# Optimization experiments

Hardware: AMD Instinct MI355X
Metric: run time of the kernel (lower is better)

The kernel has to match this reference:

```python
import jax, jax.numpy as jnp
import numpy as np

STRIDE = 1  # conv stride from __init__


def setup_inputs() -> dict:
    key = jax.random.key(0)
    k1, k2, k3 = jax.random.split(key, 3)
    prot1 = jax.random.normal(k1, (4, 1024, 8, 64), dtype=jnp.float32)
    prot2 = jax.random.normal(k2, (4, 1024, 8, 64), dtype=jnp.float32)
    # W: (no_filters, no_channels, no_dims, window_size)
    W = jax.random.normal(k3, (32, 8, 64, 7), dtype=jnp.float32)
    return {"prot1": prot1, "prot2": prot2, "W": W}


def _project(x, W, stride):
    """Fused equivalent of unfold + broadcast-mul + sum over (C, window).

    x: (N, H, C, D), W: (F, C, D, w) -> (N, F, H', D) with H' = (H - w)//stride + 1.
    This is a grouped 1D conv: D groups, each mixing C input channels into F outputs.
    """
    N, H, C, D = x.shape
    Fn, _, _, w = W.shape
    xg = jnp.transpose(x, (0, 3, 2, 1)).reshape(N, D * C, H)        # (N, D*C, H)
    Wg = jnp.transpose(W, (2, 0, 1, 3)).reshape(D * Fn, C, w)       # (D*F, C, w)
    out = jax.lax.conv_general_dilated(
        xg, Wg, window_strides=(stride,), padding='VALID',
        dimension_numbers=('NCH', 'OIH', 'NCH'), feature_group_count=D)
    Hp = out.shape[-1]
    return jnp.transpose(out.reshape(N, D, Fn, Hp), (0, 2, 3, 1))   # (N, F, H', D)


def reference(prot1, prot2, W):
    q1 = _project(prot1, W, STRIDE)   # (N, F, H1', D)
    q2 = _project(prot2, W, STRIDE)   # (N, F, H2', D)
    H1p, H2p = q1.shape[2], q2.shape[2]
    scale = jnp.sqrt(jnp.asarray(H1p * H2p, dtype=q1.dtype))
    att = jnp.einsum('nfhd,nfgd->nfhg', q1, q2) / scale             # (N, F, H1', H2')
    a = jax.nn.softmax(att, axis=3)
    p1 = jnp.einsum('nfhg,nfgd->nfhd', a, q2)                       # (N, F, H1', D)
    # NB: source does transpose(att, 2, 2) (a no-op) and multiplies the SAME
    # softmax matrix by the UPDATED p1folds; we reproduce that faithfully.
    p2 = jnp.einsum('nfhg,nfgd->nfhd', a, p1)                       # (N, F, H1', D)
    out1 = jnp.tanh(jnp.transpose(p1, (0, 2, 1, 3)))                # (N, H1', F, D)
    out2 = jnp.tanh(jnp.transpose(p2, (0, 2, 1, 3)))
    # Dropout is identity in eval mode (and dropout_p=0.0 here).
    return (out1, out2)
```

## Files before the change

### kernel.cpp

```cpp
#include <hip/hip_runtime.h>
#include <math.h>

typedef __bf16 bf16_t;
typedef bf16_t bf16x4 __attribute__((ext_vector_type(4)));
typedef bf16_t bf16x8 __attribute__((ext_vector_type(8)));
typedef float  f32x16 __attribute__((ext_vector_type(16)));

#define HH 1024
#define CC 8
#define DD 64
#define FF 32
#define WW 7
#define HP 1018
#define HPAD 1024
#define NF 128
#define QOUT (NF*HP*DD)
#define QWS ((size_t)NF*HPAD*DD)
#define SCEXP (1.442695041f/1018.f)

#if __has_builtin(__builtin_amdgcn_exp2f)
#define EXP2(x) __builtin_amdgcn_exp2f(x)
#else
#define EXP2(x) __expf((x) * 0.6931471805599453f)
#endif

__device__ __forceinline__ int vaddr(int row, int col) {
    return row*64 + ((((col>>3) ^ (row&7) ^ ((row>>2)&7)))<<3) + (col&7);
}

__global__ __launch_bounds__(256) void wprep_kernel(
    const float* __restrict__ Wt, float* __restrict__ Wp)
{
    const int idx = blockIdx.x * 256 + threadIdx.x;
    if (idx < FF*CC*DD*WW) {
        const int j = idx % WW;
        int t = idx / WW;
        const int d = t % DD; t /= DD;
        const int c = t % CC;
        const int f = t / CC;
        Wp[((f*CC + c)*WW + j)*DD + d] = Wt[idx];
    }
}

__global__ __launch_bounds__(256) void xprep_kernel(
    const float* __restrict__ x1, const float* __restrict__ x2,
    bf16_t* __restrict__ xt)
{
    __shared__ float ls[8][CC][DD+1];
    const float* x = blockIdx.z ? x2 : x1;
    bf16_t* o = xt + (size_t)blockIdx.z * (4*HH*512);
    const int n = blockIdx.y;
    const int r0 = blockIdx.x * 8;
    const int tid = threadIdx.x;

#pragma unroll
    for (int it = 0; it < 4; ++it) {
        const int i = it*256 + tid;
        const int r = i >> 7;
        const int idx = i & 127;
        const int c = idx >> 4;
        const int d0 = (idx & 15) * 4;
        float4 v = *(const float4*)&x[((size_t)(n*HH + r0 + r)*CC + c)*DD + d0];
        ls[r][c][d0+0] = v.x; ls[r][c][d0+1] = v.y;
        ls[r][c][d0+2] = v.z; ls[r][c][d0+3] = v.w;
    }
    __syncthreads();
    const int d = tid & 63;
    for (int r = (tid >> 6); r < 8; r += 4) {
        bf16_t tmp[8];
#pragma unroll
        for (int c = 0; c < CC; ++c) tmp[c] = (bf16_t)ls[r][c][d];
        *(bf16x8*)&o[((size_t)(n*HH + r0 + r)*DD + d)*CC] = *(bf16x8*)tmp;
    }
}

__global__ __launch_bounds__(256) void conv_kernel(
    const bf16_t* __restrict__ xt, const float* __restrict__ Wp,
    bf16_t* __restrict__ q1, bf16_t* __restrict__ q2)
{
    __shared__ __align__(16) bf16_t xs[22*64*8];
    const int z = blockIdx.z;
    const bf16_t* xb = xt + (size_t)z * (4*HH*512);
    bf16_t* q = z ? q2 : q1;
    const float qscale = z ? 1.0f : SCEXP;
    const int n = blockIdx.y;
    const int hb = blockIdx.x * 16;
    const int tid = threadIdx.x;

    for (int i = tid; i < 22*64; i += 256) {
        const int row = hb + (i >> 6);
        const int dd = i & 63;
        bf16x8 v = {};
        if (row < HH) v = *(const bf16x8*)&xb[((size_t)(n*HH + row)*DD + dd)*CC];
        *(bf16x8*)&xs[(size_t)i*8] = v;
    }
    __syncthreads();

    const int d = tid & 63;
    const int fq = tid >> 6;
    for (int fi = 0; fi < 8; ++fi) {
        const int f = fq*8 + fi;
        float w[CC][WW];
#pragma unroll
        for (int c = 0; c < CC; ++c)
#pragma unroll
            for (int j = 0; j < WW; ++j)
                w[c][j] = Wp[((f*CC + c)*WW + j)*DD + d];
        float acc[16];
#pragma unroll
        for (int i = 0; i < 16; ++i) acc[i] = 0.f;
#pragma unroll
        for (int rr = 0; rr < 22; ++rr) {
            bf16x8 xv8 = *(const bf16x8*)&xs[(rr*64 + d)*8];
            float xv[8];
#pragma unroll
            for (int c = 0; c < CC; ++c) xv[c] = (float)xv8[c];
#pragma unroll
            for (int j = 0; j < WW; ++j) {
                const int i = rr - j;
                if (i >= 0 && i < 16) {
#pragma unroll
                    for (int c = 0; c < CC; ++c)
                        acc[i] = fmaf(xv[c], w[c][j], acc[i]);
                }
            }
        }
#pragma unroll
        for (int i = 0; i < 16; ++i) {
            const int h = hb + i;
            const float v = (h < HP) ? acc[i] * qscale : 0.f;
            q[((size_t)(n*FF + f)*HPAD + h)*DD + d] = (bf16_t)v;
        }
    }
}

__device__ __forceinline__ float fast_tanh(float x) {
    const float t = __expf(2.f * x);
    return (t - 1.f) / (t + 1.f);
}

template<int MODE>
__global__ __launch_bounds__(256, 2) void flash(
    const bf16_t* __restrict__ q1, const bf16_t* __restrict__ q2,
    const bf16_t* __restrict__ vsrc, bf16_t* __restrict__ p1out,
    float* __restrict__ out)
{
    __shared__ __align__(16) bf16_t Vt[64*64];

    const int head = blockIdx.y;
    const int n = head >> 5, f = head & 31;
    const int tid = threadIdx.x;
    const int w = tid >> 6;
    const int lane = tid & 63;
    const int lid = lane & 31;
    const int half = lane >> 5;
    const int hb = blockIdx.x * 256 + w * 64;

    const size_t qoff = (size_t)head * HPAD * DD;
    const int vswz = (lid & 7) ^ (lid >> 2);

    const int gq = tid >> 4;
    const int dq = tid & 15;
    const int cgb = 4*((gq>>1)&1) + 8*(gq&1) + 16*(gq>>2);

    const bf16_t* vptr = (MODE == 1) ? vsrc : q2;

    bf16x8 bq1[2][4];
#pragma unroll
    for (int nt = 0; nt < 2; ++nt)
#pragma unroll
        for (int kt = 0; kt < 4; ++kt)
            bq1[nt][kt] = *(const bf16x8*)&q1[qoff + (size_t)(hb + 32*nt + lid)*DD + 16*kt + 8*half];

    bf16x8 onesb;
#pragma unroll
    for (int j = 0; j < 8; ++j) onesb[j] = (bf16_t)1.0f;

    bf16x8 aq[2][4];
#pragma unroll
    for (int mt = 0; mt < 2; ++mt)
#pragma unroll
        for (int kt = 0; kt < 4; ++kt)
            aq[mt][kt] = *(const bf16x8*)&q2[qoff + (size_t)(32*mt + lid)*DD + 16*kt + 8*half];

    bf16x4 rV[4];
#pragma unroll
    for (int i = 0; i < 4; ++i)
        rV[i] = *(const bf16x4*)&vptr[qoff + (size_t)(4*gq + i)*DD + 4*dq];

    f32x16 O[2][2] = {};
    f32x16 lO[2] = {};

    for (int g0 = 0; g0 < HPAD; g0 += 64) {
        __syncthreads();
#pragma unroll
        for (int j = 0; j < 4; ++j) {
            bf16x4 c = { rV[0][j], rV[1][j], rV[2][j], rV[3][j] };
            *(bf16x4*)&Vt[vaddr(4*dq + j, cgb)] = c;
        }
        __syncthreads();

        if (g0 + 64 < HPAD) {
#pragma unroll
            for (int i = 0; i < 4; ++i)
                rV[i] = *(const bf16x4*)&vptr[qoff + (size_t)(g0 + 64 + 4*gq + i)*DD + 4*dq];
        }

        const bool tail = (g0 + 64 > HP);

#pragma unroll
        for (int mt = 0; mt < 2; ++mt) {
            f32x16 C[2] = {};
#pragma unroll
            for (int kt = 0; kt < 4; ++kt) {
                C[0] = __builtin_amdgcn_mfma_f32_32x32x16_bf16(aq[mt][kt], bq1[0][kt], C[0], 0,0,0);
                C[1] = __builtin_amdgcn_mfma_f32_32x32x16_bf16(aq[mt][kt], bq1[1][kt], C[1], 0,0,0);
            }
            if (g0 + 64 < HPAD) {
#pragma unroll
                for (int kt = 0; kt < 4; ++kt)
                    aq[mt][kt] = *(const bf16x8*)&q2[qoff + (size_t)(g0 + 64 + 32*mt + lid)*DD + 16*kt + 8*half];
            }
            bf16x8 af[2][2];
#pragma unroll
            for (int nt = 0; nt < 2; ++nt) {
#pragma unroll
                for (int s = 0; s < 16; ++s) {
                    float e = EXP2((float)C[nt][s]);
                    if (tail) {
                        const int gg = g0 + 32*mt + (s&3) + 8*(s>>2) + 4*half;
                        if (gg >= HP) e = 0.f;
                    }
                    af[nt][s>>3][s&7] = (bf16_t)e;
                }
            }
#pragma unroll
            for (int u = 0; u < 2; ++u) {
                lO[0] = __builtin_amdgcn_mfma_f32_32x32x16_bf16(af[0][u], onesb, lO[0], 0,0,0);
                lO[1] = __builtin_amdgcn_mfma_f32_32x32x16_bf16(af[1][u], onesb, lO[1], 0,0,0);
            }
#pragma unroll
            for (int u = 0; u < 2; ++u) {
#pragma unroll
                for (int dt = 0; dt < 2; ++dt) {
                    const int chunk = (4*mt + 2*u + half) ^ vswz;
                    bf16x8 b = *(const bf16x8*)&Vt[(32*dt + lid)*64 + chunk*8];
                    O[0][dt] = __builtin_amdgcn_mfma_f32_32x32x16_bf16(af[0][u], b, O[0][dt], 0,0,0);
                    O[1][dt] = __builtin_amdgcn_mfma_f32_32x32x16_bf16(af[1][u], b, O[1][dt], 0,0,0);
                }
            }
        }
    }

#pragma unroll
    for (int ht = 0; ht < 2; ++ht) {
#pragma unroll
        for (int s = 0; s < 16; ++s) {
            const int R = (s&3) + 8*(s>>2) + 4*half;
            const int hg = hb + 32*ht + R;
            const float linv = 1.f / lO[ht][s];
#pragma unroll
            for (int dt = 0; dt < 2; ++dt) {
                const int d = 32*dt + lid;
                const float val = O[ht][dt][s] * linv;
                if (hg < HP)
                    out[(((size_t)n*HP + hg)*FF + f)*DD + d] = fast_tanh(val);
                if (MODE == 0)
                    p1out[qoff + (size_t)hg*DD + d] = (bf16_t)(hg < HP ? val : 0.f);
            }
        }
    }
}

extern "C" void kernel_launch(void* const* d_in, const int* in_sizes, int n_in,
                              void* d_out, int out_size, void* d_ws, size_t ws_size,
                              hipStream_t stream)
{
    const float* prot1 = (const float*)d_in[0];
    const float* prot2 = (const float*)d_in[1];
    const float* Wt    = (const float*)d_in[2];
    float* out = (float*)d_out;

    bf16_t* q1b = (bf16_t*)d_ws;
    bf16_t* q2b = q1b + QWS;
    bf16_t* p1b = q2b + QWS;
    float*  Wp  = (float*)(p1b + QWS);
    bf16_t* xtb = (bf16_t*)(Wp + FF*CC*DD*WW);

    wprep_kernel<<<dim3(448), 256, 0, stream>>>(Wt, Wp);
    xprep_kernel<<<dim3(HH/8, 4, 2), 256, 0, stream>>>(prot1, prot2, xtb);
    conv_kernel<<<dim3(64, 4, 2), 256, 0, stream>>>(xtb, Wp, q1b, q2b);
    flash<0><<<dim3(4, NF), 256, 0, stream>>>(q1b, q2b, q2b, p1b, out);
    flash<1><<<dim3(4, NF), 256, 0, stream>>>(q1b, q2b, p1b, p1b, out + QOUT);
}
```

Before: 248.5 us.

## Halve flash query tile per wave and pack conv FMAs into float2

The attention kernels now give each wave 32 query rows instead of 64 and launch twice as many blocks (1024 vs 512) with a higher occupancy hint, aiming to fill more CUs and overlap latency better. The trade-off is that each block now reloads the full K/V stream for half as many queries, doubling K/V traffic per output. The conv kernel is separately reworked to use paired-channel float2 multiply-adds with a matching weight layout from wprep, targeting packed FMA instructions, plus an occupancy hint and a non-unrolled filter loop.

```diff
diff --git a/kernel.cpp b/kernel.cpp
--- a/kernel.cpp
+++ b/kernel.cpp
@@ -4,6 +4,7 @@
 typedef __bf16 bf16_t;
 typedef bf16_t bf16x4 __attribute__((ext_vector_type(4)));
 typedef bf16_t bf16x8 __attribute__((ext_vector_type(8)));
+typedef float  f32x2  __attribute__((ext_vector_type(2)));
 typedef float  f32x16 __attribute__((ext_vector_type(16)));
 
 #define HH 1024
@@ -33,12 +34,13 @@
 {
     const int idx = blockIdx.x * 256 + threadIdx.x;
     if (idx < FF*CC*DD*WW) {
-        const int j = idx % WW;
-        int t = idx / WW;
-        const int d = t % DD; t /= DD;
-        const int c = t % CC;
-        const int f = t / CC;
-        Wp[((f*CC + c)*WW + j)*DD + d] = Wt[idx];
+        const int e = idx & 1;
+        int t = idx >> 1;
+        const int d = t & 63; t >>= 6;
+        const int j = t % WW; t /= WW;
+        const int cp = t & 3;
+        const int f = t >> 2;
+        Wp[idx] = Wt[((f*CC + 2*cp + e)*DD + d)*WW + j];
     }
 }
 
@@ -74,7 +76,7 @@
     }
 }
 
-__global__ __launch_bounds__(256) void conv_kernel(
+__global__ __launch_bounds__(256, 4) void conv_kernel(
     const bf16_t* __restrict__ xt, const float* __restrict__ Wp,
     bf16_t* __restrict__ q1, bf16_t* __restrict__ q2)
 {
@@ -98,37 +100,41 @@
 
     const int d = tid & 63;
     const int fq = tid >> 6;
+#pragma unroll 1
     for (int fi = 0; fi < 8; ++fi) {
         const int f = fq*8 + fi;
-        float w[CC][WW];
-#pragma unroll
-        for (int c = 0; c < CC; ++c)
+        f32x2 w2[4][WW];
+#pragma unroll
+        for (int cp = 0; cp < 4; ++cp)
 #pragma unroll
             for (int j = 0; j < WW; ++j)
-                w[c][j] = Wp[((f*CC + c)*WW + j)*DD + d];
-        float acc[16];
-#pragma unroll
-        for (int i = 0; i < 16; ++i) acc[i] = 0.f;
+                w2[cp][j] = *(const f32x2*)&Wp[((((f*4 + cp)*WW + j)*DD) + d)*2];
+        f32x2 acc2[16];
+#pragma unroll
+        for (int i = 0; i < 16; ++i) acc2[i] = (f32x2){0.f, 0.f};
 #pragma unroll
         for (int rr = 0; rr < 22; ++rr) {
             bf16x8 xv8 = *(const bf16x8*)&xs[(rr*64 + d)*8];
-            float xv[8];
-#pragma unroll
-            for (int c = 0; c < CC; ++c) xv[c] = (float)xv8[c];
+            f32x2 xv2[4];
+#pragma unroll
+            for (int cp = 0; cp < 4; ++cp) {
+                xv2[cp][0] = (float)xv8[2*cp+0];
+                xv2[cp][1] = (float)xv8[2*cp+1];
+            }
 #pragma unroll
             for (int j = 0; j < WW; ++j) {
                 const int i = rr - j;
                 if (i >= 0 && i < 16) {
 #pragma unroll
-                    for (int c = 0; c < CC; ++c)
-                        acc[i] = fmaf(xv[c], w[c][j], acc[i]);
+                    for (int cp = 0; cp < 4; ++cp)
+                        acc2[i] += xv2[cp] * w2[cp][j];
                 }
             }
         }
 #pragma unroll
         for (int i = 0; i < 16; ++i) {
             const int h = hb + i;
-            const float v = (h < HP) ? acc[i] * qscale : 0.f;
+            const float v = (h < HP) ? (acc2[i][0] + acc2[i][1]) * qscale : 0.f;
             q[((size_t)(n*FF + f)*HPAD + h)*DD + d] = (bf16_t)v;
         }
     }
@@ -140,7 +146,7 @@
 }
 
 template<int MODE>
-__global__ __launch_bounds__(256, 2) void flash(
+__global__ __launch_bounds__(256, 3) void flash(
     const bf16_t* __restrict__ q1, const bf16_t* __restrict__ q2,
     const bf16_t* __restrict__ vsrc, bf16_t* __restrict__ p1out,
     float* __restrict__ out)
@@ -154,7 +160,7 @@
     const int lane = tid & 63;
     const int lid = lane & 31;
     const int half = lane >> 5;
-    const int hb = blockIdx.x * 256 + w * 64;
+    const int hb = blockIdx.x * 128 + w * 32;
 
     const size_t qoff = (size_t)head * HPAD * DD;
     const int vswz = (lid & 7) ^ (lid >> 2);
@@ -165,12 +171,10 @@
 
     const bf16_t* vptr = (MODE == 1) ? vsrc : q2;
 
-    bf16x8 bq1[2][4];
-#pragma unroll
-    for (int nt = 0; nt < 2; ++nt)
-#pragma unroll
-        for (int kt = 0; kt < 4; ++kt)
-            bq1[nt][kt] = *(const bf16x8*)&q1[qoff + (size_t)(hb + 32*nt + lid)*DD + 16*kt + 8*half];
+    bf16x8 bq1[4];
+#pragma unroll
+    for (int kt = 0; kt < 4; ++kt)
+        bq1[kt] = *(const bf16x8*)&q1[qoff + (size_t)(hb + lid)*DD + 16*kt + 8*half];
 
     bf16x8 onesb;
 #pragma unroll
@@ -188,8 +192,8 @@
     for (int i = 0; i < 4; ++i)
         rV[i] = *(const bf16x4*)&vptr[qoff + (size_t)(4*gq + i)*DD + 4*dq];
 
-    f32x16 O[2][2] = {};
-    f32x16 lO[2] = {};
+    f32x16 O[2] = {};
+    f32x16 lO = {};
 
     for (int g0 = 0; g0 < HPAD; g0 += 64) {
         __syncthreads();
@@ -210,64 +214,53 @@
 
 #pragma unroll
         for (int mt = 0; mt < 2; ++mt) {
-            f32x16 C[2] = {};
-#pragma unroll
-            for (int kt = 0; kt < 4; ++kt) {
-                C[0] = __builtin_amdgcn_mfma_f32_32x32x16_bf16(aq[mt][kt], bq1[0][kt], C[0], 0,0,0);
-                C[1] = __builtin_amdgcn_mfma_f32_32x32x16_bf16(aq[mt][kt], bq1[1][kt], C[1], 0,0,0);
-            }
+            f32x16 C = {};
+#pragma unroll
+            for (int kt = 0; kt < 4; ++kt)
+                C = __builtin_amdgcn_mfma_f32_32x32x16_bf16(aq[mt][kt], bq1[kt], C, 0,0,0);
             if (g0 + 64 < HPAD) {
 #pragma unroll
                 for (int kt = 0; kt < 4; ++kt)
                     aq[mt][kt] = *(const bf16x8*)&q2[qoff + (size_t)(g0 + 64 + 32*mt + lid)*DD + 16*kt + 8*half];
             }
-            bf16x8 af[2][2];
-#pragma unroll
-            for (int nt = 0; nt < 2; ++nt) {
-#pragma unroll
-                for (int s = 0; s < 16; ++s) {
-                    float e = EXP2((float)C[nt][s]);
-                    if (tail) {
-                        const int gg = g0 + 32*mt + (s&3) + 8*(s>>2) + 4*half;
-                        if (gg >= HP) e = 0.f;
-                    }
-                    af[nt][s>>3][s&7] = (bf16_t)e;
+            bf16x8 af[2];
+#pragma unroll
+            for (int s = 0; s < 16; ++s) {
+                float e = EXP2((float)C[s]);
+                if (tail) {
+                    const int gg = g0 + 32*mt + (s&3) + 8*(s>>2) + 4*half;
+                    if (gg >= HP) e = 0.f;
                 }
-            }
-#pragma unroll
-            for (int u = 0; u < 2; ++u) {
-                lO[0] = __builtin_amdgcn_mfma_f32_32x32x16_bf16(af[0][u], onesb, lO[0], 0,0,0);
-                lO[1] = __builtin_amdgcn_mfma_f32_32x32x16_bf16(af[1][u], onesb, lO[1], 0,0,0);
-            }
+                af[s>>3][s&7] = (bf16_t)e;
+            }
+#pragma unroll
+            for (int u = 0; u < 2; ++u)
+                lO = __builtin_amdgcn_mfma_f32_32x32x16_bf16(af[u], onesb, lO, 0,0,0);
 #pragma unroll
             for (int u = 0; u < 2; ++u) {
 #pragma unroll
                 for (int dt = 0; dt < 2; ++dt) {
                     const int chunk = (4*mt + 2*u + half) ^ vswz;
                     bf16x8 b = *(const bf16x8*)&Vt[(32*dt + lid)*64 + chunk*8];
-                    O[0][dt] = __builtin_amdgcn_mfma_f32_32x32x16_bf16(af[0][u], b, O[0][dt], 0,0,0);
-                    O[1][dt] = __builtin_amdgcn_mfma_f32_32x32x16_bf16(af[1][u], b, O[1][dt], 0,0,0);
+                    O[dt] = __builtin_amdgcn_mfma_f32_32x32x16_bf16(af[u], b, O[dt], 0,0,0);
                 }
             }
         }
     }
 
 #pragma unroll
-    for (int ht = 0; ht < 2; ++ht) {
-#pragma unroll
-        for (int s = 0; s < 16; ++s) {
-            const int R = (s&3) + 8*(s>>2) + 4*half;
-            const int hg = hb + 32*ht + R;
-            const float linv = 1.f / lO[ht][s];
-#pragma unroll
-            for (int dt = 0; dt < 2; ++dt) {
-                const int d = 32*dt + lid;
-                const float val = O[ht][dt][s] * linv;
-                if (hg < HP)
-                    out[(((size_t)n*HP + hg)*FF + f)*DD + d] = fast_tanh(val);
-                if (MODE == 0)
-                    p1out[qoff + (size_t)hg*DD + d] = (bf16_t)(hg < HP ? val : 0.f);
-            }
+    for (int s = 0; s < 16; ++s) {
+        const int R = (s&3) + 8*(s>>2) + 4*half;
+        const int hg = hb + R;
+        const float linv = 1.f / lO[s];
+#pragma unroll
+        for (int dt = 0; dt < 2; ++dt) {
+            const int d = 32*dt + lid;
+            const float val = O[dt][s] * linv;
+            if (hg < HP)
+                out[(((size_t)n*HP + hg)*FF + f)*DD + d] = fast_tanh(val);
+            if (MODE == 0)
+                p1out[qoff + (size_t)hg*DD + d] = (bf16_t)(hg < HP ? val : 0.f);
         }
     }
 }
@@ -290,6 +283,6 @@
     wprep_kernel<<<dim3(448), 256, 0, stream>>>(Wt, Wp);
     xprep_kernel<<<dim3(HH/8, 4, 2), 256, 0, stream>>>(prot1, prot2, xtb);
     conv_kernel<<<dim3(64, 4, 2), 256, 0, stream>>>(xtb, Wp, q1b, q2b);
-    flash<0><<<dim3(4, NF), 256, 0, stream>>>(q1b, q2b, q2b, p1b, out);
-    flash<1><<<dim3(4, NF), 256, 0, stream>>>(q1b, q2b, p1b, p1b, out + QOUT);
-}
+    flash<0><<<dim3(8, NF), 256, 0, stream>>>(q1b, q2b, q2b, p1b, out);
+    flash<1><<<dim3(8, NF), 256, 0, stream>>>(q1b, q2b, p1b, p1b, out + QOUT);
+}
```

Measured after the change: 622.0 us. +150.3%, slower.
